# Kernel tuning notes

Measured on AMD Instinct MI355X. Metric: run time of the kernel, lower is better.

## Reference

```python
import jax, jax.numpy as jnp
import numpy as np

T = 20          # num_time_steps
THR = 0.05      # IafPscDelta threshold (and latency-encoding threshold)
REF = 3         # refractory_time_steps
DAMP = 1.0      # dampening_factor for surrogate gradient

@jax.custom_vjp
def spike(v_scaled):
    return (v_scaled > 0.0).astype(v_scaled.dtype)

def _spike_fwd(v_scaled):
    return spike(v_scaled), v_scaled

def _spike_bwd(v_scaled, g):
    # triangular surrogate: damp * max(0, 1 - |v_scaled|)
    return (g * DAMP * jnp.maximum(0.0, 1.0 - jnp.abs(v_scaled)),)

spike.defvjp(_spike_fwd, _spike_bwd)

def latency_encode(x):
    # snntorch.spikegen.latency(..., tau=2, threshold=0.05, normalize=True, linear=True, clip=True)
    # normalize+linear => spike_time = (T-1)*(1-x), clamped at (T-1)*(1-thr)
    tau_eff = jnp.asarray(T - 1, x.dtype)
    st = jnp.minimum(tau_eff * (1.0 - x), tau_eff * (1.0 - THR))
    t_idx = jnp.clip(jnp.round(st), 0, T - 1).astype(jnp.int32)          # [B,1,28,28]
    mask = (x >= THR).astype(x.dtype)                                     # clip=True: no spike if x < thr
    steps = jnp.arange(T, dtype=jnp.int32).reshape(T, 1, 1, 1, 1)
    return (steps == t_idx[None]).astype(x.dtype) * mask[None]            # [T,B,1,28,28]

def conv_all_steps(frames, W):
    # frames: [T,B,C,H,W]; shared weights -> batch the conv over T*B frames
    Tt, B, C, H, Wsp = frames.shape
    y = jax.lax.conv_general_dilated(frames.reshape(Tt * B, C, H, Wsp), W,
                                     window_strides=(1, 1), padding='SAME',
                                     dimension_numbers=('NCHW', 'OIHW', 'NCHW'))
    return y.reshape(Tt, B, W.shape[0], H, Wsp)

def lif(seq):
    # IafPscDelta over time: integrate (no leak), threshold, soft reset, refractory
    # seq: [T, B, ...] input currents per step
    v0 = jnp.zeros_like(seq[0])
    r0 = jnp.zeros_like(seq[0])
    def step(carry, x_t):
        v, r = carry
        v = v + x_t
        z = spike((v - THR) / THR)
        z = jnp.where(r > 0.0, jnp.zeros_like(z), z)   # refractory suppresses spikes
        v = v - z * THR                                 # perfect_reset=False -> subtract thr
        r = jnp.where(z > 0.0, jnp.full_like(r, REF), jnp.maximum(r - 1.0, 0.0))
        return (v, r), z
    _, zs = jax.lax.scan(step, (v0, r0), seq)
    return zs

def maxpool2(seq):
    Tt, B, C, H, Wsp = seq.shape
    y = jax.lax.reduce_window(seq.reshape(Tt * B, C, H, Wsp), 0.0, jax.lax.max,
                              (1, 1, 2, 2), (1, 1, 2, 2), 'VALID')
    return y.reshape(Tt, B, C, H // 2, Wsp // 2)

def setup_inputs() -> dict:
    key = jax.random.key(0)
    k1, k2, k3, k4 = jax.random.split(key, 4)
    x = jax.random.uniform(k1, (128, 1, 28, 28), dtype=jnp.float32)
    W1 = jax.random.normal(k2, (32, 1, 3, 3), dtype=jnp.float32) / np.sqrt(1 * 9)
    W2 = jax.random.normal(k3, (32, 32, 3, 3), dtype=jnp.float32) / np.sqrt(32 * 9)
    Wd = jax.random.normal(k4, (64, 32 * 7 * 7), dtype=jnp.float32) / np.sqrt(32 * 7 * 7)
    return {"x": x, "W1": W1, "W2": W2, "Wd": Wd}

def reference(x, W1, W2, Wd):
    s = latency_encode(x)                       # [T,B,1,28,28]
    h = maxpool2(lif(conv_all_steps(s, W1)))    # [T,B,32,14,14]
    h = maxpool2(lif(conv_all_steps(h, W2)))    # [T,B,32,7,7]
    Tt, B = h.shape[0], h.shape[1]
    h = h.reshape(Tt, B, -1)                    # [T,B,1568]
    h = lif(jnp.einsum('tbf,of->tbo', h, Wd))   # [T,B,64] output spikes
    return jnp.transpose(h, (1, 0, 2))          # [B,T,64]
```

## Files before the change

### kernel.cpp

```cpp
#include <hip/hip_runtime.h>

#define THRF 0.05f

__global__ void k_pre(const float* __restrict__ x, const float* __restrict__ W1,
                      const float* __restrict__ W2, const float* __restrict__ Wd,
                      unsigned* __restrict__ mIn, float* __restrict__ w1T,
                      float* __restrict__ w2T, float* __restrict__ WdT) {
  int i = blockIdx.x * blockDim.x + threadIdx.x;
  if (i >= 100352) return;
  float xv = x[i];
  float st = fminf(19.0f * (1.0f - xv), 19.0f * 0.95f);
  int t = (int)rintf(st);
  t = t < 0 ? 0 : (t > 19 ? 19 : t);
  mIn[i] = (xv >= THRF) ? (1u << t) : 0u;
  { int o = i / 1568, f = i % 1568; WdT[f * 64 + o] = Wd[i]; }
  if (i < 9216) {
    int oc = i / 288, k = i % 288, ic = k / 9, kk = k % 9;
    w2T[kk * 1024 + ic * 32 + oc] = W2[i];
  }
  if (i < 288) { int oc = i / 9, k = i % 9; w1T[k * 32 + oc] = W1[i]; }
}

__global__ __launch_bounds__(128) void k_stage1M(const unsigned* __restrict__ mIn,
                                                 const float* __restrict__ w1T,
                                                 unsigned* __restrict__ z1p) {
  __shared__ float xp[2][20 * 66];
  int lane = threadIdx.x & 63;
  int wid  = threadIdx.x >> 6;
  int gw   = blockIdx.x * 2 + wid;
  int pA = 2 * gw, pB = 2 * gw + 1;
  int bA = pA / 784, rA = pA % 784, yA = rA / 28, xA = rA % 28;
  int bB = pB / 784, rB = pB % 784, yB = rB / 28, xB = rB % 28;
  int tl = lane & 31, hiB = lane >> 5;

  unsigned mA[9], mB[9];
  for (int ky = 0; ky < 3; ++ky) {
    for (int kx = 0; kx < 3; ++kx) {
      int k = ky * 3 + kx;
      int ya = yA - 1 + ky, xa = xA - 1 + kx;
      int yb = yB - 1 + ky, xb = xB - 1 + kx;
      mA[k] = (ya >= 0 && ya < 28 && xa >= 0 && xa < 28) ? mIn[bA * 784 + ya * 28 + xa] : 0u;
      mB[k] = (yb >= 0 && yb < 28 && xb >= 0 && xb < 28) ? mIn[bB * 784 + yb * 28 + xb] : 0u;
    }
  }

  float acc[32];
#pragma unroll
  for (int o = 0; o < 32; ++o) acc[o] = 0.0f;

  for (int k = 0; k < 9; ++k) {
    unsigned long long m64 = ((unsigned long long)mB[k] << 32) | (unsigned long long)mA[k];
    float bitf = (float)((m64 >> lane) & 1ull);
    const float* wrow = w1T + k * 32;
#pragma unroll
    for (int oc = 0; oc < 32; ++oc)
      acc[oc] = fmaf(wrow[oc], bitf, acc[oc]);
  }

  if (tl < 20) {
#pragma unroll
    for (int oc = 0; oc < 32; ++oc)
      xp[wid][tl * 66 + hiB * 32 + oc] = acc[oc];
  }
  __syncthreads();

  float v = 0.0f;
  int   r = 0;
  unsigned zm = 0u;
#pragma unroll
  for (int t = 0; t < 20; ++t) {
    float c = xp[wid][t * 66 + lane];
    v += c;
    bool z = (v > THRF) && (r == 0);
    if (z) { v -= THRF; r = 3; } else if (r > 0) --r;
    if (z) zm |= 1u << t;
  }
  int p = hiB ? pB : pA;
  int b = p / 784, rr = p % 784, y = rr / 28, x = rr % 28;
  atomicOr(&z1p[((b * 14 + (y >> 1)) * 14 + (x >> 1)) * 32 + tl], zm);
}

__global__ __launch_bounds__(256) void k_stage2F(const unsigned* __restrict__ z1p,
                                                 const float* __restrict__ wT2,
                                                 const unsigned* __restrict__ zbuf,
                                                 unsigned* __restrict__ z2p) {
  __shared__ float xp[4][20 * 97];
  int lane = threadIdx.x & 63;
  int wid  = threadIdx.x >> 6;
  int gw   = blockIdx.x * 4 + wid;
  int q0 = 6 * gw;
  int  li = lane & 31;
  bool lo = lane < 32;
  int  p  = lane / 20;
  int  tl = lane - p * 20;

  int qq[6], bb[6], yy[6], xx[6];
  bool vq[6];
#pragma unroll
  for (int j = 0; j < 6; ++j) {
    int q = q0 + j;
    qq[j] = q; vq[j] = q < 25088;
    int qs = vq[j] ? q : 0;
    bb[j] = qs / 196; int rr = qs % 196; yy[j] = rr / 14; xx[j] = rr % 14;
  }

  float accA[32], accB[32];
#pragma unroll
  for (int o = 0; o < 32; ++o) { accA[o] = 0.0f; accB[o] = 0.0f; }

  for (int ky = 0; ky < 3; ++ky) {
    for (int kx = 0; kx < 3; ++kx) {
      const unsigned* cp[6];
#pragma unroll
      for (int j = 0; j < 6; ++j) {
        int y = yy[j] - 1 + ky, x = xx[j] - 1 + kx;
        bool ok = vq[j] && y >= 0 && y < 14 && x >= 0 && x < 14;
        cp[j] = ok ? (z1p + ((bb[j] * 14 + y) * 14 + x) * 32) : zbuf;
      }
      unsigned vaA = (lo ? cp[0] : cp[1])[li];
      unsigned vbA = cp[2][li];
      unsigned vaB = (lo ? cp[3] : cp[4])[li];
      unsigned vbB = cp[5][li];
      const float* wc = wT2 + (ky * 3 + kx) * 1024;
#pragma unroll 4
      for (int ic = 0; ic < 32; ++ic) {
        unsigned s0 = (unsigned)__builtin_amdgcn_readlane((int)vaA, ic);
        unsigned s1 = (unsigned)__builtin_amdgcn_readlane((int)vaA, 32 + ic);
        unsigned s2 = (unsigned)__builtin_amdgcn_readlane((int)vbA, ic);
        unsigned s3 = (unsigned)__builtin_amdgcn_readlane((int)vaB, ic);
        unsigned s4 = (unsigned)__builtin_amdgcn_readlane((int)vaB, 32 + ic);
        unsigned s5 = (unsigned)__builtin_amdgcn_readlane((int)vbB, ic);
        unsigned long long BA = (unsigned long long)s0 |
                                ((unsigned long long)s1 << 20) |
                                ((unsigned long long)s2 << 40);
        unsigned long long BB = (unsigned long long)s3 |
                                ((unsigned long long)s4 << 20) |
                                ((unsigned long long)s5 << 40);
        float bfA = (float)((BA >> lane) & 1ull);
        float bfB = (float)((BB >> lane) & 1ull);
        const float4* w4 = (const float4*)(wc + ic * 32);
#pragma unroll
        for (int j = 0; j < 8; ++j) {
          float4 w = w4[j];
          accA[4 * j + 0] = fmaf(w.x, bfA, accA[4 * j + 0]);
          accA[4 * j + 1] = fmaf(w.y, bfA, accA[4 * j + 1]);
          accA[4 * j + 2] = fmaf(w.z, bfA, accA[4 * j + 2]);
          accA[4 * j + 3] = fmaf(w.w, bfA, accA[4 * j + 3]);
          accB[4 * j + 0] = fmaf(w.x, bfB, accB[4 * j + 0]);
          accB[4 * j + 1] = fmaf(w.y, bfB, accB[4 * j + 1]);
          accB[4 * j + 2] = fmaf(w.z, bfB, accB[4 * j + 2]);
          accB[4 * j + 3] = fmaf(w.w, bfB, accB[4 * j + 3]);
        }
      }
    }
  }

#pragma unroll
  for (int s = 0; s < 2; ++s) {
    if (p < 3) {
#pragma unroll
      for (int oc = 0; oc < 32; ++oc)
        xp[wid][tl * 97 + p * 32 + oc] = (s == 0 ? accA[oc] : accB[oc]);
    }
    __syncthreads();
    for (int pass = 0; pass < 2; ++pass) {
      int n = lane + 64 * pass;
      if (n < 96) {
        int pp = n >> 5;
        int oc = n & 31;
        int j  = 3 * s + pp;
        if (vq[j]) {
          float v = 0.0f;
          int   r = 0;
          unsigned zm = 0u;
#pragma unroll
          for (int t = 0; t < 20; ++t) {
            float c = xp[wid][t * 97 + n];
            v += c;
            bool z = (v > THRF) && (r == 0);
            if (z) { v -= THRF; r = 3; } else if (r > 0) --r;
            if (z) zm |= 1u << t;
          }
          atomicOr(&z2p[bb[j] * 1568 + oc * 49 + (yy[j] >> 1) * 7 + (xx[j] >> 1)], zm);
        }
      }
    }
    __syncthreads();
  }
}

__global__ __launch_bounds__(256) void k_denseF(const unsigned* __restrict__ z2p,
                                                const float* __restrict__ WdT,
                                                float* __restrict__ out) {
  int lane = threadIdx.x & 63;
  int wid  = threadIdx.x >> 6;
  int gw   = blockIdx.x * 4 + wid;
  if (gw >= 128 * 22) return;
  int b  = gw / 22, og = gw % 22;
  int p  = lane / 20;
  int t  = lane - p * 20;
  int o  = og * 3 + p;
  bool live = (p < 3) && (o < 64);
  int osafe = live ? o : 63;
  const unsigned* zb = z2p + b * 1568;

  unsigned mA[16], mB[16];
  float    wA[16], wB[16];
#pragma unroll
  for (int u = 0; u < 16; ++u) { mA[u] = zb[u]; wA[u] = WdT[u * 64 + osafe]; }

  float acc = 0.0f;
  for (int f0 = 0; f0 < 1568; f0 += 32) {
#pragma unroll
    for (int u = 0; u < 16; ++u) {
      int fn = f0 + 16 + u;
      mB[u] = zb[fn]; wB[u] = WdT[fn * 64 + osafe];
    }
#pragma unroll
    for (int u = 0; u < 16; ++u) {
      float bitf = (float)((mA[u] >> t) & 1u);
      acc = fmaf(wA[u], bitf, acc);
    }
    if (f0 + 32 < 1568) {
#pragma unroll
      for (int u = 0; u < 16; ++u) {
        int fn = f0 + 32 + u;
        mA[u] = zb[fn]; wA[u] = WdT[fn * 64 + osafe];
      }
    }
#pragma unroll
    for (int u = 0; u < 16; ++u) {
      float bitf = (float)((mB[u] >> t) & 1u);
      acc = fmaf(wB[u], bitf, acc);
    }
  }

  float v = 0.0f;
  int   r = 0;
  unsigned zm = 0u;
#pragma unroll
  for (int tt = 0; tt < 20; ++tt) {
    float c = __shfl(acc, p * 20 + tt, 64);
    v += c;
    bool z = (v > THRF) && (r == 0);
    if (z) { v -= THRF; r = 3; } else if (r > 0) --r;
    if (z) zm |= 1u << tt;
  }
  if (live) out[(b * 20 + t) * 64 + o] = ((zm >> t) & 1u) ? 1.0f : 0.0f;
}

extern "C" void kernel_launch(void* const* d_in, const int* in_sizes, int n_in,
                              void* d_out, int out_size, void* d_ws, size_t ws_size,
                              hipStream_t stream) {
  const float* x  = (const float*)d_in[0];
  const float* W1 = (const float*)d_in[1];
  const float* W2 = (const float*)d_in[2];
  const float* Wd = (const float*)d_in[3];
  float* out = (float*)d_out;

  char* ws = (char*)d_ws;
  unsigned* mIn  = (unsigned*)ws;
  unsigned* z1p  = (unsigned*)(ws + 655360);
  unsigned* z2p  = (unsigned*)(ws + 3866624);
  unsigned* zbuf = (unsigned*)(ws + 4669440);
  float*    w1T  = (float*)(ws + 4669568);
  float*    w2T  = (float*)(ws + 4670720);
  float*    WdT  = (float*)(ws + 4707584);

  k_pre<<<dim3(392), dim3(256), 0, stream>>>(x, W1, W2, Wd, mIn, w1T, w2T, WdT);
  hipMemsetAsync(ws + 655360, 0, 3211264 + 802816 + 128, stream);
  k_stage1M<<<dim3(25088), dim3(128), 0, stream>>>(mIn, w1T, z1p);
  k_stage2F<<<dim3(1046), dim3(256), 0, stream>>>(z1p, w2T, zbuf, z2p);
  k_denseF<<<dim3(704), dim3(256), 0, stream>>>(z2p, WdT, out);
}
```

Before: 311.5 us.

## Halve per-wave positions in conv2 stage and double-buffer weights in LDS

The second conv+LIF kernel now handles 3 output positions per wave instead of 6. That halves the accumulator registers from 64 to 32 floats and doubles the grid. Each 3x3 tap's weight slice is staged into double-buffered shared memory, and the next tap's spike words are prefetched while the current tap is computed. The LIF epilogue is simplified to a per-position pass. The aim is higher occupancy and overlap of loads with FMAs, at the cost of twice as many weight reads overall, a block barrier per tap, and redundant LIF work in the upper half-wave.

```diff
diff --git a/kernel.cpp b/kernel.cpp
--- a/kernel.cpp
+++ b/kernel.cpp
@@ -80,112 +80,105 @@
   atomicOr(&z1p[((b * 14 + (y >> 1)) * 14 + (x >> 1)) * 32 + tl], zm);
 }
 
-__global__ __launch_bounds__(256) void k_stage2F(const unsigned* __restrict__ z1p,
+__global__ __launch_bounds__(256) void k_stage2G(const unsigned* __restrict__ z1p,
                                                  const float* __restrict__ wT2,
                                                  const unsigned* __restrict__ zbuf,
                                                  unsigned* __restrict__ z2p) {
-  __shared__ float xp[4][20 * 97];
-  int lane = threadIdx.x & 63;
-  int wid  = threadIdx.x >> 6;
+  __shared__ float4 wbuf4[2][256];
+  __shared__ float  xp[4][20 * 33];
+  int tid  = threadIdx.x;
+  int lane = tid & 63;
+  int wid  = tid >> 6;
   int gw   = blockIdx.x * 4 + wid;
-  int q0 = 6 * gw;
+  int q0 = 3 * gw;
+
+  int bb[3], yy[3], xx[3];
+  bool vq[3];
+#pragma unroll
+  for (int j = 0; j < 3; ++j) {
+    int q = q0 + j;
+    vq[j] = q < 25088;
+    int qs = vq[j] ? q : 0;
+    bb[j] = qs / 196; int rr = qs % 196; yy[j] = rr / 14; xx[j] = rr % 14;
+  }
+
   int  li = lane & 31;
   bool lo = lane < 32;
   int  p  = lane / 20;
   int  tl = lane - p * 20;
 
-  int qq[6], bb[6], yy[6], xx[6];
-  bool vq[6];
-#pragma unroll
-  for (int j = 0; j < 6; ++j) {
-    int q = q0 + j;
-    qq[j] = q; vq[j] = q < 25088;
-    int qs = vq[j] ? q : 0;
-    bb[j] = qs / 196; int rr = qs % 196; yy[j] = rr / 14; xx[j] = rr % 14;
-  }
-
-  float accA[32], accB[32];
-#pragma unroll
-  for (int o = 0; o < 32; ++o) { accA[o] = 0.0f; accB[o] = 0.0f; }
-
-  for (int ky = 0; ky < 3; ++ky) {
-    for (int kx = 0; kx < 3; ++kx) {
-      const unsigned* cp[6];
-#pragma unroll
-      for (int j = 0; j < 6; ++j) {
-        int y = yy[j] - 1 + ky, x = xx[j] - 1 + kx;
-        bool ok = vq[j] && y >= 0 && y < 14 && x >= 0 && x < 14;
-        cp[j] = ok ? (z1p + ((bb[j] * 14 + y) * 14 + x) * 32) : zbuf;
-      }
-      unsigned vaA = (lo ? cp[0] : cp[1])[li];
-      unsigned vbA = cp[2][li];
-      unsigned vaB = (lo ? cp[3] : cp[4])[li];
-      unsigned vbB = cp[5][li];
-      const float* wc = wT2 + (ky * 3 + kx) * 1024;
+  float acc[32];
+#pragma unroll
+  for (int o = 0; o < 32; ++o) acc[o] = 0.0f;
+
+  auto cptr = [&](int cell, const unsigned*& c0, const unsigned*& c1,
+                  const unsigned*& c2) {
+    int ky = cell / 3, kx = cell % 3;
+    const unsigned* cp[3];
+#pragma unroll
+    for (int j = 0; j < 3; ++j) {
+      int y = yy[j] - 1 + ky, x = xx[j] - 1 + kx;
+      bool ok = vq[j] && y >= 0 && y < 14 && x >= 0 && x < 14;
+      cp[j] = ok ? (z1p + ((bb[j] * 14 + y) * 14 + x) * 32) : zbuf;
+    }
+    c0 = cp[0]; c1 = cp[1]; c2 = cp[2];
+  };
+
+  wbuf4[0][tid] = *(const float4*)(wT2 + tid * 4);
+  const unsigned *c0, *c1, *c2;
+  cptr(0, c0, c1, c2);
+  unsigned va = (lo ? c0 : c1)[li];
+  unsigned vb = c2[li];
+  __syncthreads();
+
+  for (int cell = 0; cell < 9; ++cell) {
+    int cur = cell & 1;
+    unsigned va_n = 0u, vb_n = 0u;
+    if (cell + 1 < 9) {
+      wbuf4[cur ^ 1][tid] = *(const float4*)(wT2 + (cell + 1) * 1024 + tid * 4);
+      const unsigned *n0, *n1, *n2;
+      cptr(cell + 1, n0, n1, n2);
+      va_n = (lo ? n0 : n1)[li];
+      vb_n = n2[li];
+    }
+    const float* wc = (const float*)wbuf4[cur];
 #pragma unroll 4
-      for (int ic = 0; ic < 32; ++ic) {
-        unsigned s0 = (unsigned)__builtin_amdgcn_readlane((int)vaA, ic);
-        unsigned s1 = (unsigned)__builtin_amdgcn_readlane((int)vaA, 32 + ic);
-        unsigned s2 = (unsigned)__builtin_amdgcn_readlane((int)vbA, ic);
-        unsigned s3 = (unsigned)__builtin_amdgcn_readlane((int)vaB, ic);
-        unsigned s4 = (unsigned)__builtin_amdgcn_readlane((int)vaB, 32 + ic);
-        unsigned s5 = (unsigned)__builtin_amdgcn_readlane((int)vbB, ic);
-        unsigned long long BA = (unsigned long long)s0 |
-                                ((unsigned long long)s1 << 20) |
-                                ((unsigned long long)s2 << 40);
-        unsigned long long BB = (unsigned long long)s3 |
-                                ((unsigned long long)s4 << 20) |
-                                ((unsigned long long)s5 << 40);
-        float bfA = (float)((BA >> lane) & 1ull);
-        float bfB = (float)((BB >> lane) & 1ull);
-        const float4* w4 = (const float4*)(wc + ic * 32);
-#pragma unroll
-        for (int j = 0; j < 8; ++j) {
-          float4 w = w4[j];
-          accA[4 * j + 0] = fmaf(w.x, bfA, accA[4 * j + 0]);
-          accA[4 * j + 1] = fmaf(w.y, bfA, accA[4 * j + 1]);
-          accA[4 * j + 2] = fmaf(w.z, bfA, accA[4 * j + 2]);
-          accA[4 * j + 3] = fmaf(w.w, bfA, accA[4 * j + 3]);
-          accB[4 * j + 0] = fmaf(w.x, bfB, accB[4 * j + 0]);
-          accB[4 * j + 1] = fmaf(w.y, bfB, accB[4 * j + 1]);
-          accB[4 * j + 2] = fmaf(w.z, bfB, accB[4 * j + 2]);
-          accB[4 * j + 3] = fmaf(w.w, bfB, accB[4 * j + 3]);
-        }
-      }
-    }
-  }
-
-#pragma unroll
-  for (int s = 0; s < 2; ++s) {
-    if (p < 3) {
+    for (int ic = 0; ic < 32; ++ic) {
+      unsigned s0 = (unsigned)__builtin_amdgcn_readlane((int)va, ic);
+      unsigned s1 = (unsigned)__builtin_amdgcn_readlane((int)va, 32 + ic);
+      unsigned s2 = (unsigned)__builtin_amdgcn_readlane((int)vb, ic);
+      unsigned mm = (p == 0) ? s0 : ((p == 1) ? s1 : s2);
+      float bitf = (float)((mm >> tl) & 1u);
+      const float* wrow = wc + ic * 32;
 #pragma unroll
       for (int oc = 0; oc < 32; ++oc)
-        xp[wid][tl * 97 + p * 32 + oc] = (s == 0 ? accA[oc] : accB[oc]);
-    }
+        acc[oc] = fmaf(wrow[oc], bitf, acc[oc]);
+    }
+    va = va_n; vb = vb_n;
     __syncthreads();
-    for (int pass = 0; pass < 2; ++pass) {
-      int n = lane + 64 * pass;
-      if (n < 96) {
-        int pp = n >> 5;
-        int oc = n & 31;
-        int j  = 3 * s + pp;
-        if (vq[j]) {
-          float v = 0.0f;
-          int   r = 0;
-          unsigned zm = 0u;
-#pragma unroll
-          for (int t = 0; t < 20; ++t) {
-            float c = xp[wid][t * 97 + n];
-            v += c;
-            bool z = (v > THRF) && (r == 0);
-            if (z) { v -= THRF; r = 3; } else if (r > 0) --r;
-            if (z) zm |= 1u << t;
-          }
-          atomicOr(&z2p[bb[j] * 1568 + oc * 49 + (yy[j] >> 1) * 7 + (xx[j] >> 1)], zm);
-        }
-      }
-    }
-    __syncthreads();
+  }
+
+  float* xw = xp[wid];
+#pragma unroll
+  for (int j = 0; j < 3; ++j) {
+    if (p == j) {
+#pragma unroll
+      for (int oc = 0; oc < 32; ++oc) xw[tl * 33 + oc] = acc[oc];
+    }
+    int oc = lane & 31;
+    float v = 0.0f;
+    int   r = 0;
+    unsigned zm = 0u;
+#pragma unroll
+    for (int t = 0; t < 20; ++t) {
+      float c = xw[t * 33 + oc];
+      v += c;
+      bool z = (v > THRF) && (r == 0);
+      if (z) { v -= THRF; r = 3; } else if (r > 0) --r;
+      if (z) zm |= 1u << t;
+    }
+    if (lane < 32 && vq[j])
+      atomicOr(&z2p[bb[j] * 1568 + oc * 49 + (yy[j] >> 1) * 7 + (xx[j] >> 1)], zm);
   }
 }
 
@@ -270,6 +263,6 @@
   k_pre<<<dim3(392), dim3(256), 0, stream>>>(x, W1, W2, Wd, mIn, w1T, w2T, WdT);
   hipMemsetAsync(ws + 655360, 0, 3211264 + 802816 + 128, stream);
   k_stage1M<<<dim3(25088), dim3(128), 0, stream>>>(mIn, w1T, z1p);
-  k_stage2F<<<dim3(1046), dim3(256), 0, stream>>>(z1p, w2T, zbuf, z2p);
+  k_stage2G<<<dim3(2091), dim3(256), 0, stream>>>(z1p, w2T, zbuf, z2p);
   k_denseF<<<dim3(704), dim3(256), 0, stream>>>(z2p, WdT, out);
 }
```

New measurement: 322.9 us. 3.7% more time.

## Run stage-2 conv as single-wave blocks with next-tap spike prefetch

Applied to the files above, without the earlier changes.

Replaces the 4-wave stage-2 conv/LIF kernel with a one-wavefront-per-block version of the same computation. Each block now loads the spike words for the next 3x3 tap while it computes the current tap. Because a block is a single wave, both __syncthreads barriers around the LDS transpose are removed. The output base indices are precomputed so the epilogue does less address arithmetic. The tradeoffs are higher register pressure from the prefetched values and the (64,4) launch bounds. Dropping the barriers also relies on LDS accesses staying ordered within a wave.

```diff
diff --git a/kernel.cpp b/kernel.cpp
--- a/kernel.cpp
+++ b/kernel.cpp
@@ -80,79 +80,94 @@
   atomicOr(&z1p[((b * 14 + (y >> 1)) * 14 + (x >> 1)) * 32 + tl], zm);
 }
 
-__global__ __launch_bounds__(256) void k_stage2F(const unsigned* __restrict__ z1p,
-                                                 const float* __restrict__ wT2,
-                                                 const unsigned* __restrict__ zbuf,
-                                                 unsigned* __restrict__ z2p) {
-  __shared__ float xp[4][20 * 97];
-  int lane = threadIdx.x & 63;
-  int wid  = threadIdx.x >> 6;
-  int gw   = blockIdx.x * 4 + wid;
-  int q0 = 6 * gw;
+__global__ __launch_bounds__(64, 4) void k_stage2K(const unsigned* __restrict__ z1p,
+                                                   const float* __restrict__ wT2,
+                                                   const unsigned* __restrict__ zbuf,
+                                                   unsigned* __restrict__ z2p) {
+  __shared__ float xw[20 * 97];
+  int lane = threadIdx.x;
+  int gw   = blockIdx.x;
+  int q0   = 6 * gw;
+
+  int bb[6], yy[6], xx[6], outIdx[6];
+  bool vq[6];
+#pragma unroll
+  for (int j = 0; j < 6; ++j) {
+    int q = q0 + j;
+    vq[j] = q < 25088;
+    int qs = vq[j] ? q : 0;
+    bb[j] = qs / 196; int rr = qs % 196; yy[j] = rr / 14; xx[j] = rr % 14;
+    outIdx[j] = bb[j] * 1568 + (yy[j] >> 1) * 7 + (xx[j] >> 1);
+  }
+
   int  li = lane & 31;
   bool lo = lane < 32;
   int  p  = lane / 20;
   int  tl = lane - p * 20;
 
-  int qq[6], bb[6], yy[6], xx[6];
-  bool vq[6];
-#pragma unroll
-  for (int j = 0; j < 6; ++j) {
-    int q = q0 + j;
-    qq[j] = q; vq[j] = q < 25088;
-    int qs = vq[j] ? q : 0;
-    bb[j] = qs / 196; int rr = qs % 196; yy[j] = rr / 14; xx[j] = rr % 14;
-  }
-
   float accA[32], accB[32];
 #pragma unroll
   for (int o = 0; o < 32; ++o) { accA[o] = 0.0f; accB[o] = 0.0f; }
 
-  for (int ky = 0; ky < 3; ++ky) {
-    for (int kx = 0; kx < 3; ++kx) {
-      const unsigned* cp[6];
-#pragma unroll
-      for (int j = 0; j < 6; ++j) {
-        int y = yy[j] - 1 + ky, x = xx[j] - 1 + kx;
-        bool ok = vq[j] && y >= 0 && y < 14 && x >= 0 && x < 14;
-        cp[j] = ok ? (z1p + ((bb[j] * 14 + y) * 14 + x) * 32) : zbuf;
+  auto cptr = [&](int cell, const unsigned* cp[6]) {
+    int ky = cell / 3, kx = cell % 3;
+#pragma unroll
+    for (int j = 0; j < 6; ++j) {
+      int y = yy[j] - 1 + ky, x = xx[j] - 1 + kx;
+      bool ok = vq[j] && y >= 0 && y < 14 && x >= 0 && x < 14;
+      cp[j] = ok ? (z1p + ((bb[j] * 14 + y) * 14 + x) * 32) : zbuf;
+    }
+  };
+
+  const unsigned* cp[6];
+  cptr(0, cp);
+  unsigned vaA = (lo ? cp[0] : cp[1])[li];
+  unsigned vbA = cp[2][li];
+  unsigned vaB = (lo ? cp[3] : cp[4])[li];
+  unsigned vbB = cp[5][li];
+
+  for (int cell = 0; cell < 9; ++cell) {
+    unsigned vaA_n = 0u, vbA_n = 0u, vaB_n = 0u, vbB_n = 0u;
+    if (cell + 1 < 9) {
+      const unsigned* np[6];
+      cptr(cell + 1, np);
+      vaA_n = (lo ? np[0] : np[1])[li];
+      vbA_n = np[2][li];
+      vaB_n = (lo ? np[3] : np[4])[li];
+      vbB_n = np[5][li];
+    }
+    const float* wc = wT2 + cell * 1024;
+#pragma unroll 4
+    for (int ic = 0; ic < 32; ++ic) {
+      unsigned s0 = (unsigned)__builtin_amdgcn_readlane((int)vaA, ic);
+      unsigned s1 = (unsigned)__builtin_amdgcn_readlane((int)vaA, 32 + ic);
+      unsigned s2 = (unsigned)__builtin_amdgcn_readlane((int)vbA, ic);
+      unsigned s3 = (unsigned)__builtin_amdgcn_readlane((int)vaB, ic);
+      unsigned s4 = (unsigned)__builtin_amdgcn_readlane((int)vaB, 32 + ic);
+      unsigned s5 = (unsigned)__builtin_amdgcn_readlane((int)vbB, ic);
+      unsigned long long BA = (unsigned long long)s0 |
+                              ((unsigned long long)s1 << 20) |
+                              ((unsigned long long)s2 << 40);
+      unsigned long long BB = (unsigned long long)s3 |
+                              ((unsigned long long)s4 << 20) |
+                              ((unsigned long long)s5 << 40);
+      float bfA = (float)((BA >> lane) & 1ull);
+      float bfB = (float)((BB >> lane) & 1ull);
+      const float4* w4 = (const float4*)(wc + ic * 32);
+#pragma unroll
+      for (int j = 0; j < 8; ++j) {
+        float4 w = w4[j];
+        accA[4 * j + 0] = fmaf(w.x, bfA, accA[4 * j + 0]);
+        accA[4 * j + 1] = fmaf(w.y, bfA, accA[4 * j + 1]);
+        accA[4 * j + 2] = fmaf(w.z, bfA, accA[4 * j + 2]);
+        accA[4 * j + 3] = fmaf(w.w, bfA, accA[4 * j + 3]);
+        accB[4 * j + 0] = fmaf(w.x, bfB, accB[4 * j + 0]);
+        accB[4 * j + 1] = fmaf(w.y, bfB, accB[4 * j + 1]);
+        accB[4 * j + 2] = fmaf(w.z, bfB, accB[4 * j + 2]);
+        accB[4 * j + 3] = fmaf(w.w, bfB, accB[4 * j + 3]);
       }
-      unsigned vaA = (lo ? cp[0] : cp[1])[li];
-      unsigned vbA = cp[2][li];
-      unsigned vaB = (lo ? cp[3] : cp[4])[li];
-      unsigned vbB = cp[5][li];
-      const float* wc = wT2 + (ky * 3 + kx) * 1024;
-#pragma unroll 4
-      for (int ic = 0; ic < 32; ++ic) {
-        unsigned s0 = (unsigned)__builtin_amdgcn_readlane((int)vaA, ic);
-        unsigned s1 = (unsigned)__builtin_amdgcn_readlane((int)vaA, 32 + ic);
-        unsigned s2 = (unsigned)__builtin_amdgcn_readlane((int)vbA, ic);
-        unsigned s3 = (unsigned)__builtin_amdgcn_readlane((int)vaB, ic);
-        unsigned s4 = (unsigned)__builtin_amdgcn_readlane((int)vaB, 32 + ic);
-        unsigned s5 = (unsigned)__builtin_amdgcn_readlane((int)vbB, ic);
-        unsigned long long BA = (unsigned long long)s0 |
-                                ((unsigned long long)s1 << 20) |
-                                ((unsigned long long)s2 << 40);
-        unsigned long long BB = (unsigned long long)s3 |
-                                ((unsigned long long)s4 << 20) |
-                                ((unsigned long long)s5 << 40);
-        float bfA = (float)((BA >> lane) & 1ull);
-        float bfB = (float)((BB >> lane) & 1ull);
-        const float4* w4 = (const float4*)(wc + ic * 32);
-#pragma unroll
-        for (int j = 0; j < 8; ++j) {
-          float4 w = w4[j];
-          accA[4 * j + 0] = fmaf(w.x, bfA, accA[4 * j + 0]);
-          accA[4 * j + 1] = fmaf(w.y, bfA, accA[4 * j + 1]);
-          accA[4 * j + 2] = fmaf(w.z, bfA, accA[4 * j + 2]);
-          accA[4 * j + 3] = fmaf(w.w, bfA, accA[4 * j + 3]);
-          accB[4 * j + 0] = fmaf(w.x, bfB, accB[4 * j + 0]);
-          accB[4 * j + 1] = fmaf(w.y, bfB, accB[4 * j + 1]);
-          accB[4 * j + 2] = fmaf(w.z, bfB, accB[4 * j + 2]);
-          accB[4 * j + 3] = fmaf(w.w, bfB, accB[4 * j + 3]);
-        }
-      }
-    }
+    }
+    vaA = vaA_n; vbA = vbA_n; vaB = vaB_n; vbB = vbB_n;
   }
 
 #pragma unroll
@@ -160,32 +175,33 @@
     if (p < 3) {
 #pragma unroll
       for (int oc = 0; oc < 32; ++oc)
-        xp[wid][tl * 97 + p * 32 + oc] = (s == 0 ? accA[oc] : accB[oc]);
-    }
-    __syncthreads();
+        xw[tl * 97 + p * 32 + oc] = (s == 0 ? accA[oc] : accB[oc]);
+    }
+#pragma unroll
     for (int pass = 0; pass < 2; ++pass) {
       int n = lane + 64 * pass;
       if (n < 96) {
         int pp = n >> 5;
         int oc = n & 31;
-        int j  = 3 * s + pp;
-        if (vq[j]) {
+        bool val  = (pp == 0) ? vq[3 * s] : ((pp == 1) ? vq[3 * s + 1] : vq[3 * s + 2]);
+        int  base = (pp == 0) ? outIdx[3 * s]
+                  : ((pp == 1) ? outIdx[3 * s + 1] : outIdx[3 * s + 2]);
+        if (val) {
           float v = 0.0f;
           int   r = 0;
           unsigned zm = 0u;
 #pragma unroll
           for (int t = 0; t < 20; ++t) {
-            float c = xp[wid][t * 97 + n];
+            float c = xw[t * 97 + n];
             v += c;
             bool z = (v > THRF) && (r == 0);
             if (z) { v -= THRF; r = 3; } else if (r > 0) --r;
             if (z) zm |= 1u << t;
           }
-          atomicOr(&z2p[bb[j] * 1568 + oc * 49 + (yy[j] >> 1) * 7 + (xx[j] >> 1)], zm);
+          atomicOr(&z2p[base + oc * 49], zm);
         }
       }
     }
-    __syncthreads();
   }
 }
 
@@ -270,6 +286,6 @@
   k_pre<<<dim3(392), dim3(256), 0, stream>>>(x, W1, W2, Wd, mIn, w1T, w2T, WdT);
   hipMemsetAsync(ws + 655360, 0, 3211264 + 802816 + 128, stream);
   k_stage1M<<<dim3(25088), dim3(128), 0, stream>>>(mIn, w1T, z1p);
-  k_stage2F<<<dim3(1046), dim3(256), 0, stream>>>(z1p, w2T, zbuf, z2p);
+  k_stage2K<<<dim3(4182), dim3(64), 0, stream>>>(z1p, w2T, zbuf, z2p);
   k_denseF<<<dim3(704), dim3(256), 0, stream>>>(z2p, WdT, out);
 }
```

Result: slower. 404.6 us (+29.9%).
